# Kernel tuning notes

Measured on AMD Instinct MI355X. Metric: run time of the kernel, lower is better.

The kernel has to match this reference:

```python
import jax, jax.numpy as jnp
import numpy as np

N_NODES = 100000
N_EDGES = 1600000
IN_FEATS = 256
OUT_FEATS = 128


def setup_inputs() -> dict:
    key = jax.random.key(0)
    k1, k2, k3, k4 = jax.random.split(key, 4)
    feat = jax.random.normal(k1, (N_NODES, IN_FEATS), dtype=jnp.float32)
    # Glorot-uniform-like weight
    limit = np.sqrt(6.0 / (IN_FEATS + OUT_FEATS)).astype(np.float32)
    weight = jax.random.uniform(k2, (IN_FEATS, OUT_FEATS), dtype=jnp.float32,
                                minval=-limit, maxval=limit)
    bias = jnp.zeros((OUT_FEATS,), dtype=jnp.float32)
    src = jax.random.randint(k3, (N_EDGES,), 0, N_NODES, dtype=jnp.int32)
    dst = jax.random.randint(k4, (N_EDGES,), 0, N_NODES, dtype=jnp.int32)
    return {"feat": feat, "weight": weight, "bias": bias, "src": src, "dst": dst}


def reference(feat, weight, bias, src, dst):
    n = feat.shape[0]
    # in-degree per node (edges point src -> dst), clipped to >= 1
    deg = jax.ops.segment_sum(jnp.ones_like(dst, dtype=feat.dtype), dst,
                              num_segments=n)
    norm = jnp.clip(deg, 1.0, None) ** -0.5          # [N]
    norm = norm[:, None]                             # [N, 1]
    h = feat * norm                                  # src-side normalization
    # in_feats > out_feats: project first, then aggregate (cheaper messages)
    h = h @ weight                                   # [N, out]
    agg = jax.ops.segment_sum(h[src], dst, num_segments=n)  # sparse sum-aggregate
    rst = agg * norm + bias                          # dst-side norm + bias
    return rst
```

## Files before the change

### kernel.cpp

```cpp
#include <hip/hip_runtime.h>

#define IN_F 256
#define OUT_F 128
#define BSH 7
#define BNODES 128
#define MAXBUCK 1024
#define BIN1A_BLOCKS 256
#define BIN1B_BLOCKS 256

typedef short bf16x8 __attribute__((ext_vector_type(8)));
typedef float f32x4 __attribute__((ext_vector_type(4)));
typedef unsigned short us8 __attribute__((ext_vector_type(8)));

__device__ inline unsigned short f2bf(float x) {
    union { float f; unsigned u; } v; v.f = x;
    unsigned r = v.u + 0x7FFFu + ((v.u >> 16) & 1u);
    return (unsigned short)(r >> 16);
}
__device__ inline float bf2f(unsigned short x) {
    union { unsigned u; float f; } v; v.u = ((unsigned)x) << 16;
    return v.f;
}

__global__ __launch_bounds__(256) void prep_kernel(const float* __restrict__ W,
                                                   unsigned short* __restrict__ Wt,
                                                   const int* __restrict__ dst,
                                                   int* __restrict__ bhist,
                                                   int n_edges, int nbuck) {
    if ((int)blockIdx.x < BIN1A_BLOCKS) {
        __shared__ int hist[MAXBUCK];
        const int tid = threadIdx.x;
        const int chunk = (n_edges + BIN1A_BLOCKS - 1) / BIN1A_BLOCKS;
        const int lo = blockIdx.x * chunk;
        const int hi = min(lo + chunk, n_edges);

        for (int i = tid; i < MAXBUCK; i += 256) hist[i] = 0;
        __syncthreads();
        for (int e = lo + tid; e < hi; e += 256)
            atomicAdd(&hist[dst[e] >> BSH], 1);
        __syncthreads();
        for (int i = tid; i < nbuck; i += 256) {
            int c = hist[i];
            if (c) atomicAdd(&bhist[i], c);
        }
    } else {
        int n = blockIdx.x - BIN1A_BLOCKS;
        int k = threadIdx.x;
        Wt[n * IN_F + k] = f2bf(W[k * OUT_F + n]);
    }
}

__global__ __launch_bounds__(1024) void scanb_kernel(const int* __restrict__ bhist,
                                                     int* __restrict__ bstart,
                                                     int* __restrict__ gcur,
                                                     int* __restrict__ rstart,
                                                     int nbuck, int n_nodes) {
    __shared__ int sh[1024];
    int tid = threadIdx.x;
    int v = (tid < nbuck) ? bhist[tid] : 0;
    sh[tid] = v;
    __syncthreads();
    #pragma unroll
    for (int off = 1; off < 1024; off <<= 1) {
        int t = (tid >= off) ? sh[tid - off] : 0;
        __syncthreads();
        sh[tid] += t;
        __syncthreads();
    }
    int ex = sh[tid] - v;
    if (tid < nbuck) { bstart[tid] = ex; gcur[tid] = ex; }
    if (tid == 1023) {
        bstart[nbuck] = sh[1023];
        rstart[n_nodes] = sh[1023];
    }
}

__global__ __launch_bounds__(256) void bin1b_kernel(const int* __restrict__ src,
                                                    const int* __restrict__ dst,
                                                    int* __restrict__ gcur,
                                                    unsigned* __restrict__ ebuf,
                                                    int n_edges, int nbuck) {
    __shared__ int hist[MAXBUCK];
    __shared__ int lbase[MAXBUCK];
    const int tid = threadIdx.x;
    const int chunk = (n_edges + BIN1B_BLOCKS - 1) / BIN1B_BLOCKS;
    const int lo = blockIdx.x * chunk;
    const int hi = min(lo + chunk, n_edges);

    for (int i = tid; i < nbuck; i += 256) hist[i] = 0;
    __syncthreads();
    for (int e = lo + tid; e < hi; e += 256)
        atomicAdd(&hist[dst[e] >> BSH], 1);
    __syncthreads();
    for (int i = tid; i < nbuck; i += 256) {
        int c = hist[i];
        lbase[i] = (c > 0) ? atomicAdd(&gcur[i], c) : 0;
        hist[i] = 0;
    }
    __syncthreads();
    for (int e = lo + tid; e < hi; e += 256) {
        int d = dst[e];
        int bkt = d >> BSH;
        int off = atomicAdd(&hist[bkt], 1);
        ebuf[lbase[bkt] + off] = ((unsigned)src[e] << BSH) | (unsigned)(d & (BNODES - 1));
    }
}

__global__ __launch_bounds__(1024) void gemm_mfma(const float* __restrict__ feat,
                                                  const unsigned short* __restrict__ Wt,
                                                  unsigned short* __restrict__ h,
                                                  int n_nodes) {
    __shared__ unsigned short Bs[OUT_F * IN_F];

    const int tid  = threadIdx.x;
    const int wave = tid >> 6;
    const int lane = tid & 63;
    const int r0   = (blockIdx.x * 16 + wave) * 16;
    const int lrow = lane & 15;
    const int g    = lane >> 4;
    const int kgrp = g * 8;

    {
        const f32x4* srcv = reinterpret_cast<const f32x4*>(Wt);
        f32x4* dstv = reinterpret_cast<f32x4*>(Bs);
        #pragma unroll
        for (int i = 0; i < 4; ++i) {
            int c   = tid + i * 1024;
            int row = c >> 5;
            int col = c & 31;
            dstv[c] = srcv[row * 32 + (col ^ (row & 7))];
        }
    }

    const int row  = r0 + lrow;
    const int rowc = (row < n_nodes) ? row : (n_nodes - 1);
    const float* arow = feat + (size_t)rowc * IN_F;

    __syncthreads();

    f32x4 acc[8];
    #pragma unroll
    for (int n = 0; n < 8; ++n) acc[n] = (f32x4){0.f, 0.f, 0.f, 0.f};

    const bf16x8* bsv = reinterpret_cast<const bf16x8*>(Bs);

    #pragma unroll
    for (int k0 = 0; k0 < IN_F / 32; ++k0) {
        const f32x4 a0 = *reinterpret_cast<const f32x4*>(arow + k0 * 32 + kgrp);
        const f32x4 a1 = *reinterpret_cast<const f32x4*>(arow + k0 * 32 + kgrp + 4);
        bf16x8 afr;
        afr[0] = (short)f2bf(a0[0]);
        afr[1] = (short)f2bf(a0[1]);
        afr[2] = (short)f2bf(a0[2]);
        afr[3] = (short)f2bf(a0[3]);
        afr[4] = (short)f2bf(a1[0]);
        afr[5] = (short)f2bf(a1[1]);
        afr[6] = (short)f2bf(a1[2]);
        afr[7] = (short)f2bf(a1[3]);
        #pragma unroll
        for (int n = 0; n < 8; ++n) {
            const int brow = n * 16 + lrow;
            bf16x8 bfr = bsv[brow * 32 + ((k0 * 4 + g) ^ (brow & 7))];
            acc[n] = __builtin_amdgcn_mfma_f32_16x16x32_bf16(afr, bfr, acc[n], 0, 0, 0);
        }
    }

    const int orow0 = r0 + g * 4;
    #pragma unroll
    for (int n = 0; n < 8; ++n) {
        #pragma unroll
        for (int j = 0; j < 4; ++j) {
            int orow = orow0 + j;
            if (orow < n_nodes)
                h[(size_t)orow * OUT_F + n * 16 + lrow] = f2bf(acc[n][j]);
        }
    }
}

__global__ __launch_bounds__(256) void bin2_kernel(const unsigned* __restrict__ ebuf,
                                                   const int* __restrict__ bstart,
                                                   int* __restrict__ rstart,
                                                   float* __restrict__ norm,
                                                   int* __restrict__ eidx,
                                                   int n_nodes) {
    __shared__ int lcnt[BNODES];
    __shared__ int lex[BNODES];
    const int tid = threadIdx.x;
    const int node0 = blockIdx.x << BSH;
    const int e0 = bstart[blockIdx.x];
    const int e1 = bstart[blockIdx.x + 1];

    if (tid < BNODES) lcnt[tid] = 0;
    __syncthreads();
    for (int e = e0 + tid; e < e1; e += 256)
        atomicAdd(&lcnt[ebuf[e] & (BNODES - 1)], 1);
    __syncthreads();

    int own = (tid < BNODES) ? lcnt[tid] : 0;
    if (tid < BNODES) lex[tid] = own;
    __syncthreads();
    #pragma unroll
    for (int off = 1; off < BNODES; off <<= 1) {
        int t = (tid >= off && tid < BNODES) ? lex[tid - off] : 0;
        __syncthreads();
        if (tid < BNODES) lex[tid] += t;
        __syncthreads();
    }
    if (tid < BNODES) {
        int ex = lex[tid] - own;
        lex[tid] = ex;
        int g = node0 + tid;
        if (g <= n_nodes) rstart[g] = e0 + ex;
        if (g < n_nodes) {
            float d = (float)own;
            if (d < 1.0f) d = 1.0f;
            norm[g] = 1.0f / sqrtf(d);
        }
        lcnt[tid] = 0;
    }
    __syncthreads();

    for (int e = e0 + tid; e < e1; e += 256) {
        unsigned pk = ebuf[e];
        int dl = pk & (BNODES - 1);
        int pos = atomicAdd(&lcnt[dl], 1);
        eidx[e0 + lex[dl] + pos] = (int)(pk >> BSH);
    }
}

__global__ __launch_bounds__(256) void agg_kernel(const unsigned short* __restrict__ h,
                                                  const int* __restrict__ eidx,
                                                  const int* __restrict__ rstart,
                                                  const float* __restrict__ norm,
                                                  const float* __restrict__ bias,
                                                  float* __restrict__ out,
                                                  int n_nodes) {
    const int wave = threadIdx.x >> 6;
    const int lane = threadIdx.x & 63;
    const int grp  = lane >> 4;
    const int gl   = lane & 15;
    const int node = blockIdx.x * 4 + wave;
    if (node >= n_nodes) return;

    const int start = rstart[node];
    const int cnt   = rstart[node + 1] - start;
    const unsigned short* __restrict__ hb = h + gl * 8;

    float acc[8] = {0.f, 0.f, 0.f, 0.f, 0.f, 0.f, 0.f, 0.f};

    for (int base = 0; base < cnt; base += 64) {
        const int rem = min(64, cnt - base);
        int   ev = (lane < rem) ? eidx[start + base + lane] : 0;
        float nv = (lane < rem) ? norm[ev] : 0.f;

        int j = 0;
        for (; j + 16 <= rem; j += 16) {
            int   s0 = __shfl(ev, j + grp);
            int   s1 = __shfl(ev, j + grp + 4);
            int   s2 = __shfl(ev, j + grp + 8);
            int   s3 = __shfl(ev, j + grp + 12);
            float n0 = __shfl(nv, j + grp);
            float n1 = __shfl(nv, j + grp + 4);
            float n2 = __shfl(nv, j + grp + 8);
            float n3 = __shfl(nv, j + grp + 12);
            us8 v0 = *reinterpret_cast<const us8*>(hb + (size_t)s0 * OUT_F);
            us8 v1 = *reinterpret_cast<const us8*>(hb + (size_t)s1 * OUT_F);
            us8 v2 = *reinterpret_cast<const us8*>(hb + (size_t)s2 * OUT_F);
            us8 v3 = *reinterpret_cast<const us8*>(hb + (size_t)s3 * OUT_F);
            #pragma unroll
            for (int q = 0; q < 8; ++q) {
                acc[q] += bf2f(v0[q]) * n0 + bf2f(v1[q]) * n1
                        + bf2f(v2[q]) * n2 + bf2f(v3[q]) * n3;
            }
        }
        for (; j < rem; j += 4) {
            int   je = j + grp;
            int   jc = min(je, rem - 1);
            int   s  = __shfl(ev, jc);
            float nm = __shfl(nv, jc);
            if (je >= rem) nm = 0.f;
            us8 v = *reinterpret_cast<const us8*>(hb + (size_t)s * OUT_F);
            #pragma unroll
            for (int q = 0; q < 8; ++q)
                acc[q] += bf2f(v[q]) * nm;
        }
    }

    #pragma unroll
    for (int q = 0; q < 8; ++q) {
        acc[q] += __shfl_xor(acc[q], 16);
        acc[q] += __shfl_xor(acc[q], 32);
    }

    if (grp == 0) {
        const float nd = norm[node];
        const float4 b0 = *reinterpret_cast<const float4*>(bias + gl * 8);
        const float4 b1 = *reinterpret_cast<const float4*>(bias + gl * 8 + 4);
        float4 r0, r1;
        r0.x = acc[0] * nd + b0.x;
        r0.y = acc[1] * nd + b0.y;
        r0.z = acc[2] * nd + b0.z;
        r0.w = acc[3] * nd + b0.w;
        r1.x = acc[4] * nd + b1.x;
        r1.y = acc[5] * nd + b1.y;
        r1.z = acc[6] * nd + b1.z;
        r1.w = acc[7] * nd + b1.w;
        float* o = out + (size_t)node * OUT_F + gl * 8;
        *reinterpret_cast<float4*>(o)     = r0;
        *reinterpret_cast<float4*>(o + 4) = r1;
    }
}

extern "C" void kernel_launch(void* const* d_in, const int* in_sizes, int n_in,
                              void* d_out, int out_size, void* d_ws, size_t ws_size,
                              hipStream_t stream) {
    const float* feat   = (const float*)d_in[0];
    const float* weight = (const float*)d_in[1];
    const float* bias   = (const float*)d_in[2];
    const int*   src    = (const int*)d_in[3];
    const int*   dst    = (const int*)d_in[4];
    float* out = (float*)d_out;

    const int n_nodes = in_sizes[0] / IN_F;
    const int n_edges = in_sizes[3];
    const int nbuck   = (n_nodes + BNODES - 1) >> BSH;
    const int gemm_blocks = (n_nodes + 255) / 256;

    char* ws = (char*)d_ws;
    size_t off = 0;
    auto alloc = [&](size_t bytes) {
        char* p = ws + off;
        off += (bytes + 15) & ~(size_t)15;
        return p;
    };
    unsigned short* h  = (unsigned short*)alloc((size_t)n_nodes * OUT_F * 2);
    float* norm        = (float*)alloc((size_t)n_nodes * 4);
    int*   rstart      = (int*)alloc(((size_t)n_nodes + 1) * 4);
    int*   bhist       = (int*)alloc(MAXBUCK * 4);
    int*   bstart      = (int*)alloc((MAXBUCK + 1) * 4);
    int*   gcur        = (int*)alloc(MAXBUCK * 4);
    unsigned short* Wt = (unsigned short*)alloc((size_t)OUT_F * IN_F * 2);
    unsigned* ebuf     = (unsigned*)alloc((size_t)n_edges * 4);
    int*   eidx        = (int*)alloc((size_t)n_edges * 4);

    hipMemsetAsync(bhist, 0, MAXBUCK * sizeof(int), stream);
    prep_kernel<<<BIN1A_BLOCKS + OUT_F, 256, 0, stream>>>(weight, Wt, dst, bhist,
                                                          n_edges, nbuck);
    scanb_kernel<<<1, 1024, 0, stream>>>(bhist, bstart, gcur, rstart, nbuck, n_nodes);
    bin1b_kernel<<<BIN1B_BLOCKS, 256, 0, stream>>>(src, dst, gcur, ebuf, n_edges, nbuck);
    gemm_mfma<<<gemm_blocks, 1024, 0, stream>>>(feat, Wt, h, n_nodes);
    bin2_kernel<<<nbuck, 256, 0, stream>>>(ebuf, bstart, rstart, norm, eidx, n_nodes);
    agg_kernel<<<(n_nodes + 3) / 4, 256, 0, stream>>>(h, eidx, rstart, norm, bias, out, n_nodes);
}
```

Measured before the change: 156.2 us.

## Fuse edge binning into GEMM launch and replicate bucket scan per block

The single-block bucket scan kernel is removed. Each binning block and each bin2 block now recomputes the bucket prefix sum from the histogram itself. The bin1b pass is merged into the GEMM launch as extra heterogeneous 1024-thread blocks, so edge scattering can run alongside the MFMA projection. This removes two kernel launches and a serial dependency. In exchange, the scan work is duplicated in every block, and the binning blocks reserve a 64KB shared buffer they mostly do not use, which limits their occupancy.

```diff
diff --git a/kernel.cpp b/kernel.cpp
--- a/kernel.cpp
+++ b/kernel.cpp
@@ -50,145 +50,167 @@
     }
 }
 
-__global__ __launch_bounds__(1024) void scanb_kernel(const int* __restrict__ bhist,
-                                                     int* __restrict__ bstart,
-                                                     int* __restrict__ gcur,
-                                                     int* __restrict__ rstart,
-                                                     int nbuck, int n_nodes) {
-    __shared__ int sh[1024];
-    int tid = threadIdx.x;
-    int v = (tid < nbuck) ? bhist[tid] : 0;
-    sh[tid] = v;
-    __syncthreads();
-    #pragma unroll
-    for (int off = 1; off < 1024; off <<= 1) {
-        int t = (tid >= off) ? sh[tid - off] : 0;
-        __syncthreads();
-        sh[tid] += t;
-        __syncthreads();
-    }
-    int ex = sh[tid] - v;
-    if (tid < nbuck) { bstart[tid] = ex; gcur[tid] = ex; }
-    if (tid == 1023) {
-        bstart[nbuck] = sh[1023];
-        rstart[n_nodes] = sh[1023];
-    }
-}
-
-__global__ __launch_bounds__(256) void bin1b_kernel(const int* __restrict__ src,
-                                                    const int* __restrict__ dst,
-                                                    int* __restrict__ gcur,
-                                                    unsigned* __restrict__ ebuf,
-                                                    int n_edges, int nbuck) {
-    __shared__ int hist[MAXBUCK];
-    __shared__ int lbase[MAXBUCK];
-    const int tid = threadIdx.x;
-    const int chunk = (n_edges + BIN1B_BLOCKS - 1) / BIN1B_BLOCKS;
-    const int lo = blockIdx.x * chunk;
-    const int hi = min(lo + chunk, n_edges);
-
-    for (int i = tid; i < nbuck; i += 256) hist[i] = 0;
-    __syncthreads();
-    for (int e = lo + tid; e < hi; e += 256)
-        atomicAdd(&hist[dst[e] >> BSH], 1);
-    __syncthreads();
-    for (int i = tid; i < nbuck; i += 256) {
-        int c = hist[i];
-        lbase[i] = (c > 0) ? atomicAdd(&gcur[i], c) : 0;
-        hist[i] = 0;
-    }
-    __syncthreads();
-    for (int e = lo + tid; e < hi; e += 256) {
-        int d = dst[e];
-        int bkt = d >> BSH;
-        int off = atomicAdd(&hist[bkt], 1);
-        ebuf[lbase[bkt] + off] = ((unsigned)src[e] << BSH) | (unsigned)(d & (BNODES - 1));
-    }
-}
-
-__global__ __launch_bounds__(1024) void gemm_mfma(const float* __restrict__ feat,
-                                                  const unsigned short* __restrict__ Wt,
-                                                  unsigned short* __restrict__ h,
-                                                  int n_nodes) {
-    __shared__ unsigned short Bs[OUT_F * IN_F];
-
-    const int tid  = threadIdx.x;
-    const int wave = tid >> 6;
-    const int lane = tid & 63;
-    const int r0   = (blockIdx.x * 16 + wave) * 16;
-    const int lrow = lane & 15;
-    const int g    = lane >> 4;
-    const int kgrp = g * 8;
-
-    {
-        const f32x4* srcv = reinterpret_cast<const f32x4*>(Wt);
-        f32x4* dstv = reinterpret_cast<f32x4*>(Bs);
-        #pragma unroll
-        for (int i = 0; i < 4; ++i) {
-            int c   = tid + i * 1024;
-            int row = c >> 5;
-            int col = c & 31;
-            dstv[c] = srcv[row * 32 + (col ^ (row & 7))];
-        }
-    }
-
-    const int row  = r0 + lrow;
-    const int rowc = (row < n_nodes) ? row : (n_nodes - 1);
-    const float* arow = feat + (size_t)rowc * IN_F;
-
-    __syncthreads();
-
-    f32x4 acc[8];
-    #pragma unroll
-    for (int n = 0; n < 8; ++n) acc[n] = (f32x4){0.f, 0.f, 0.f, 0.f};
-
-    const bf16x8* bsv = reinterpret_cast<const bf16x8*>(Bs);
-
-    #pragma unroll
-    for (int k0 = 0; k0 < IN_F / 32; ++k0) {
-        const f32x4 a0 = *reinterpret_cast<const f32x4*>(arow + k0 * 32 + kgrp);
-        const f32x4 a1 = *reinterpret_cast<const f32x4*>(arow + k0 * 32 + kgrp + 4);
-        bf16x8 afr;
-        afr[0] = (short)f2bf(a0[0]);
-        afr[1] = (short)f2bf(a0[1]);
-        afr[2] = (short)f2bf(a0[2]);
-        afr[3] = (short)f2bf(a0[3]);
-        afr[4] = (short)f2bf(a1[0]);
-        afr[5] = (short)f2bf(a1[1]);
-        afr[6] = (short)f2bf(a1[2]);
-        afr[7] = (short)f2bf(a1[3]);
+__global__ __launch_bounds__(1024) void gemm_bin_kernel(
+        const float* __restrict__ feat, const unsigned short* __restrict__ Wt,
+        unsigned short* __restrict__ h, int n_nodes,
+        const int* __restrict__ src, const int* __restrict__ dst,
+        const int* __restrict__ bhist, int* __restrict__ gcur0,
+        unsigned* __restrict__ ebuf, int n_edges, int nbuck) {
+
+    __shared__ __align__(16) char smem[65536];
+
+    if ((int)blockIdx.x < BIN1B_BLOCKS) {
+        int* scanv = (int*)smem;
+        int* hist  = scanv + MAXBUCK;
+        int* lbase = hist + MAXBUCK;
+        const int tid = threadIdx.x;
+        const int chunk = (n_edges + BIN1B_BLOCKS - 1) / BIN1B_BLOCKS;
+        const int lo = blockIdx.x * chunk;
+        const int hi = min(lo + chunk, n_edges);
+
+        int own = (tid < nbuck) ? bhist[tid] : 0;
+        scanv[tid] = own;
+        __syncthreads();
+        #pragma unroll
+        for (int off = 1; off < MAXBUCK; off <<= 1) {
+            int t = (tid >= off) ? scanv[tid - off] : 0;
+            __syncthreads();
+            scanv[tid] += t;
+            __syncthreads();
+        }
+        int bstart_t = scanv[tid] - own;
+        __syncthreads();
+        scanv[tid] = bstart_t;
+        hist[tid] = 0;
+        __syncthreads();
+
+        for (int e = lo + tid; e < hi; e += 1024)
+            atomicAdd(&hist[dst[e] >> BSH], 1);
+        __syncthreads();
+        if (tid < nbuck) {
+            int c = hist[tid];
+            lbase[tid] = (c > 0) ? (scanv[tid] + atomicAdd(&gcur0[tid], c)) : 0;
+            hist[tid] = 0;
+        }
+        __syncthreads();
+        for (int e = lo + tid; e < hi; e += 1024) {
+            int d = dst[e];
+            int bkt = d >> BSH;
+            int off = atomicAdd(&hist[bkt], 1);
+            ebuf[lbase[bkt] + off] = ((unsigned)src[e] << BSH) | (unsigned)(d & (BNODES - 1));
+        }
+    } else {
+        unsigned short* Bs = (unsigned short*)smem;
+
+        const int tid  = threadIdx.x;
+        const int wave = tid >> 6;
+        const int lane = tid & 63;
+        const int gb   = blockIdx.x - BIN1B_BLOCKS;
+        const int r0   = (gb * 16 + wave) * 16;
+        const int lrow = lane & 15;
+        const int g    = lane >> 4;
+        const int kgrp = g * 8;
+
+        {
+            const f32x4* srcv = reinterpret_cast<const f32x4*>(Wt);
+            f32x4* dstv = reinterpret_cast<f32x4*>(Bs);
+            #pragma unroll
+            for (int i = 0; i < 4; ++i) {
+                int c   = tid + i * 1024;
+                int row = c >> 5;
+                int col = c & 31;
+                dstv[c] = srcv[row * 32 + (col ^ (row & 7))];
+            }
+        }
+
+        const int row  = r0 + lrow;
+        const int rowc = (row < n_nodes) ? row : (n_nodes - 1);
+        const float* arow = feat + (size_t)rowc * IN_F;
+
+        __syncthreads();
+
+        f32x4 acc[8];
+        #pragma unroll
+        for (int n = 0; n < 8; ++n) acc[n] = (f32x4){0.f, 0.f, 0.f, 0.f};
+
+        const bf16x8* bsv = reinterpret_cast<const bf16x8*>(Bs);
+
+        #pragma unroll
+        for (int k0 = 0; k0 < IN_F / 32; ++k0) {
+            const f32x4 a0 = *reinterpret_cast<const f32x4*>(arow + k0 * 32 + kgrp);
+            const f32x4 a1 = *reinterpret_cast<const f32x4*>(arow + k0 * 32 + kgrp + 4);
+            bf16x8 afr;
+            afr[0] = (short)f2bf(a0[0]);
+            afr[1] = (short)f2bf(a0[1]);
+            afr[2] = (short)f2bf(a0[2]);
+            afr[3] = (short)f2bf(a0[3]);
+            afr[4] = (short)f2bf(a1[0]);
+            afr[5] = (short)f2bf(a1[1]);
+            afr[6] = (short)f2bf(a1[2]);
+            afr[7] = (short)f2bf(a1[3]);
+            #pragma unroll
+            for (int n = 0; n < 8; ++n) {
+                const int brow = n * 16 + lrow;
+                bf16x8 bfr = bsv[brow * 32 + ((k0 * 4 + g) ^ (brow & 7))];
+                acc[n] = __builtin_amdgcn_mfma_f32_16x16x32_bf16(afr, bfr, acc[n], 0, 0, 0);
+            }
+        }
+
+        const int orow0 = r0 + g * 4;
         #pragma unroll
         for (int n = 0; n < 8; ++n) {
-            const int brow = n * 16 + lrow;
-            bf16x8 bfr = bsv[brow * 32 + ((k0 * 4 + g) ^ (brow & 7))];
-            acc[n] = __builtin_amdgcn_mfma_f32_16x16x32_bf16(afr, bfr, acc[n], 0, 0, 0);
-        }
-    }
-
-    const int orow0 = r0 + g * 4;
-    #pragma unroll
-    for (int n = 0; n < 8; ++n) {
-        #pragma unroll
-        for (int j = 0; j < 4; ++j) {
-            int orow = orow0 + j;
-            if (orow < n_nodes)
-                h[(size_t)orow * OUT_F + n * 16 + lrow] = f2bf(acc[n][j]);
+            #pragma unroll
+            for (int j = 0; j < 4; ++j) {
+                int orow = orow0 + j;
+                if (orow < n_nodes)
+                    h[(size_t)orow * OUT_F + n * 16 + lrow] = f2bf(acc[n][j]);
+            }
         }
     }
 }
 
 __global__ __launch_bounds__(256) void bin2_kernel(const unsigned* __restrict__ ebuf,
-                                                   const int* __restrict__ bstart,
+                                                   const int* __restrict__ bhist,
                                                    int* __restrict__ rstart,
                                                    float* __restrict__ norm,
                                                    int* __restrict__ eidx,
-                                                   int n_nodes) {
+                                                   int n_nodes, int nbuck) {
+    __shared__ int bs[MAXBUCK];
     __shared__ int lcnt[BNODES];
     __shared__ int lex[BNODES];
     const int tid = threadIdx.x;
     const int node0 = blockIdx.x << BSH;
-    const int e0 = bstart[blockIdx.x];
-    const int e1 = bstart[blockIdx.x + 1];
+
+    {
+        int v[4], s = 0;
+        #pragma unroll
+        for (int j = 0; j < 4; ++j) {
+            int idx = tid * 4 + j;
+            v[j] = (idx < nbuck) ? bhist[idx] : 0;
+            s += v[j];
+        }
+        lexinit:;
+        __shared__ int sh[256];
+        sh[tid] = s;
+        __syncthreads();
+        #pragma unroll
+        for (int off = 1; off < 256; off <<= 1) {
+            int t = (tid >= off) ? sh[tid - off] : 0;
+            __syncthreads();
+            sh[tid] += t;
+            __syncthreads();
+        }
+        int ex = sh[tid] - s;
+        #pragma unroll
+        for (int j = 0; j < 4; ++j) {
+            bs[tid * 4 + j] = ex;
+            ex += v[j];
+        }
+    }
+    __syncthreads();
+
+    const int e0 = bs[blockIdx.x];
+    const int e1 = e0 + bhist[blockIdx.x];
 
     if (tid < BNODES) lcnt[tid] = 0;
     __syncthreads();
@@ -336,19 +358,18 @@
     unsigned short* h  = (unsigned short*)alloc((size_t)n_nodes * OUT_F * 2);
     float* norm        = (float*)alloc((size_t)n_nodes * 4);
     int*   rstart      = (int*)alloc(((size_t)n_nodes + 1) * 4);
-    int*   bhist       = (int*)alloc(MAXBUCK * 4);
-    int*   bstart      = (int*)alloc((MAXBUCK + 1) * 4);
-    int*   gcur        = (int*)alloc(MAXBUCK * 4);
+    int*   bhist       = (int*)alloc(2 * MAXBUCK * 4);
+    int*   gcur0       = bhist + MAXBUCK;
     unsigned short* Wt = (unsigned short*)alloc((size_t)OUT_F * IN_F * 2);
     unsigned* ebuf     = (unsigned*)alloc((size_t)n_edges * 4);
     int*   eidx        = (int*)alloc((size_t)n_edges * 4);
 
-    hipMemsetAsync(bhist, 0, MAXBUCK * sizeof(int), stream);
+    hipMemsetAsync(bhist, 0, 2 * MAXBUCK * sizeof(int), stream);
     prep_kernel<<<BIN1A_BLOCKS + OUT_F, 256, 0, stream>>>(weight, Wt, dst, bhist,
                                                           n_edges, nbuck);
-    scanb_kernel<<<1, 1024, 0, stream>>>(bhist, bstart, gcur, rstart, nbuck, n_nodes);
-    bin1b_kernel<<<BIN1B_BLOCKS, 256, 0, stream>>>(src, dst, gcur, ebuf, n_edges, nbuck);
-    gemm_mfma<<<gemm_blocks, 1024, 0, stream>>>(feat, Wt, h, n_nodes);
-    bin2_kernel<<<nbuck, 256, 0, stream>>>(ebuf, bstart, rstart, norm, eidx, n_nodes);
+    gemm_bin_kernel<<<BIN1B_BLOCKS + gemm_blocks, 1024, 0, stream>>>(
+        feat, Wt, h, n_nodes, src, dst, bhist, gcur0, ebuf, n_edges, nbuck);
+    bin2_kernel<<<nbuck, 256, 0, stream>>>(ebuf, bhist, rstart, norm, eidx,
+                                           n_nodes, nbuck);
     agg_kernel<<<(n_nodes + 3) / 4, 256, 0, stream>>>(h, eidx, rstart, norm, bias, out, n_nodes);
 }
```

Measured after the change: 146.3 us. 6.3% less time.
